# Optimization experiments

Hardware: AMD Instinct MI355X
Metric: run time of the kernel (lower is better)

## Reference

```python
import jax, jax.numpy as jnp
import numpy as np

D_MODEL = 1024
N_HEADS = 16
HEAD_DIM = D_MODEL // N_HEADS
B, S = 4, 2048


def setup_inputs() -> dict:
    key = jax.random.key(0)
    ks = jax.random.split(key, 11)
    scale = 1.0 / np.sqrt(D_MODEL)
    inp = {
        "query": jax.random.normal(ks[0], (B, S, D_MODEL), jnp.float32),
        "key": jax.random.normal(ks[1], (B, S, D_MODEL), jnp.float32),
        "value": jax.random.normal(ks[2], (B, S, D_MODEL), jnp.float32),
        "Wq": jax.random.normal(ks[3], (D_MODEL, D_MODEL), jnp.float32) * scale,
        "bq": jnp.zeros((D_MODEL,), jnp.float32),
        "Wk": jax.random.normal(ks[4], (D_MODEL, D_MODEL), jnp.float32) * scale,
        "bk": jnp.zeros((D_MODEL,), jnp.float32),
        "Wv": jax.random.normal(ks[5], (D_MODEL, D_MODEL), jnp.float32) * scale,
        "bv": jnp.zeros((D_MODEL,), jnp.float32),
        "Wo": jax.random.normal(ks[6], (D_MODEL, D_MODEL), jnp.float32) * scale,
        "bo": jnp.zeros((D_MODEL,), jnp.float32),
    }
    return inp


def _split_heads(x):
    b, s, _ = x.shape
    return x.reshape(b, s, N_HEADS, HEAD_DIM).transpose(0, 2, 1, 3)  # b h s d


def reference(query, key, value, Wq, bq, Wk, bk, Wv, bv, Wo, bo):
    Q = _split_heads(query @ Wq.T + bq)
    K = _split_heads(key @ Wk.T + bk)
    V = _split_heads(value @ Wv.T + bv)
    scale = 1.0 / jnp.sqrt(jnp.float32(HEAD_DIM))
    energy = jnp.einsum("bhqd,bhkd->bhqk", Q, K) * scale  # full N x N scores
    attn = jax.nn.softmax(energy, axis=-1)
    x = jnp.einsum("bhqk,bhkd->bhqd", attn, V)
    x = x.transpose(0, 2, 1, 3).reshape(query.shape[0], -1, D_MODEL)
    return x @ Wo.T + bo
```

## Files before the change

### kernel.cpp

```cpp
#include <hip/hip_runtime.h>
#include <cstdint>
#include <cstddef>


typedef unsigned short u16;
typedef unsigned u32;
typedef short short8 __attribute__((ext_vector_type(8)));
typedef __bf16 bf16x8 __attribute__((ext_vector_type(8)));
typedef float f32x4 __attribute__((ext_vector_type(4)));
typedef float f32x16 __attribute__((ext_vector_type(16)));
typedef unsigned short u16x4 __attribute__((ext_vector_type(4)));
typedef unsigned u32x2 __attribute__((ext_vector_type(2)));
typedef unsigned u32x4 __attribute__((ext_vector_type(4)));
typedef int iv2 __attribute__((ext_vector_type(2)));

__device__ __forceinline__ u16 f2bf(float f) {
  unsigned u = __builtin_bit_cast(unsigned, f);
  u += 0x7fffu + ((u >> 16) & 1u);
  return (u16)(u >> 16);
}
__device__ __forceinline__ bf16x8 bc8(short8 v) { return __builtin_bit_cast(bf16x8, v); }
__device__ __forceinline__ u32 pk_bf16(float a, float b) {
  u32 r;
  asm("v_cvt_pk_bf16_f32 %0, %1, %2" : "=v"(r) : "v"(a), "v"(b));
  return r;
}
__device__ __forceinline__ void gload16(const u16* g, u16* l) {
  __builtin_amdgcn_global_load_lds((const __attribute__((address_space(1))) void*)g,
                                   (__attribute__((address_space(3))) void*)l, 16, 0, 0);
}

__global__ __launch_bounds__(256) void cvt_all(const float* __restrict__ q,
                                               const float* __restrict__ k,
                                               const float* __restrict__ v,
                                               const float* __restrict__ wq,
                                               const float* __restrict__ wk,
                                               const float* __restrict__ wv,
                                               const float* __restrict__ wo,
                                               u16* __restrict__ xq, u16* __restrict__ xk,
                                               u16* __restrict__ xv, u16* __restrict__ wqb,
                                               u16* __restrict__ wkb, u16* __restrict__ wvb,
                                               u16* __restrict__ wob) {
  const size_t i4 = (size_t)blockIdx.x * 256 + threadIdx.x;
  const size_t A4 = 1ull << 21, W4 = 1ull << 18;
  const float* s;
  u16* d;
  size_t off;
  if (i4 < 3 * A4) {
    const int r = (int)(i4 >> 21);
    off = i4 & (A4 - 1);
    s = r == 0 ? q : (r == 1 ? k : v);
    d = r == 0 ? xq : (r == 1 ? xk : xv);
  } else {
    const size_t t = i4 - 3 * A4;
    const int r = (int)(t >> 18);
    off = t & (W4 - 1);
    s = r == 0 ? wq : (r == 1 ? wk : (r == 2 ? wv : wo));
    d = r == 0 ? wqb : (r == 1 ? wkb : (r == 2 ? wvb : wob));
  }
  const f32x4 a = ((const f32x4*)s)[off];
  u32x2 o = {pk_bf16(a[0], a[1]), pk_bf16(a[2], a[3])};
  ((u32x2*)d)[off] = o;
}

__device__ __forceinline__ bf16x8 ldf(const u16* buf, int row, int g) {
  return bc8(*(const short8*)(buf + row * 32 + g * 8));
}

__device__ __forceinline__ void gemm_core(u16* lds, const u16* __restrict__ A,
                                          const u16* __restrict__ Bw,
                                          const float* __restrict__ bias,
                                          void* __restrict__ C, int mode, float oscale) {
  const int t = threadIdx.x;
  const int w = t >> 6, l = t & 63, g = l >> 4, m = l & 15;
  const int wr = w >> 1, wc = w & 1;
  const int m0 = blockIdx.x * 128, n0 = blockIdx.y * 256;
  const u16* gA = A + (size_t)m0 * 1024;
  const u16* gB = Bw + (size_t)n0 * 1024;

  f32x4 acc[4][8];
  const f32x4 z = {0.f, 0.f, 0.f, 0.f};
#pragma unroll
  for (int i = 0; i < 4; ++i)
#pragma unroll
    for (int j = 0; j < 8; ++j) acc[i][j] = z;

#pragma unroll
  for (int tt = 0; tt < 2; ++tt) {
    u16* sA = lds + tt * 12288;
    u16* sB = sA + 4096;
    const int ko = tt * 32;
#pragma unroll
    for (int r = 0; r < 2; ++r) {
      const int c = r * 256 + t;
      gload16(gA + (size_t)(c >> 2) * 1024 + (c & 3) * 8 + ko, sA + c * 8);
    }
#pragma unroll
    for (int r = 0; r < 4; ++r) {
      const int c = r * 256 + t;
      gload16(gB + (size_t)(c >> 2) * 1024 + (c & 3) * 8 + ko, sB + c * 8);
    }
  }
  asm volatile("s_waitcnt vmcnt(6)" ::: "memory");
  __builtin_amdgcn_s_barrier();

  bf16x8 af[4], bfr[8];
  int cb = 0;
  for (int tt = 0; tt < 32; ++tt) {
    u16* bA = lds + cb * 12288;
    u16* bB = bA + 4096;
    const int sbi = (cb == 0) ? 2 : cb - 1;
    u16* sA = lds + sbi * 12288;
    u16* sB = sA + 4096;
    const int ko = (tt + 2) * 32;
    const bool st = tt < 30;

    af[0] = ldf(bA, wr * 64 + m, g);
    af[1] = ldf(bA, wr * 64 + 16 + m, g);
#pragma unroll
    for (int j = 0; j < 4; ++j) bfr[j] = ldf(bB, wc * 128 + j * 16 + m, g);
    if (st) {
#pragma unroll
      for (int r = 0; r < 2; ++r) {
        const int c = r * 256 + t;
        gload16(gA + (size_t)(c >> 2) * 1024 + (c & 3) * 8 + ko, sA + c * 8);
      }
    }
    __builtin_amdgcn_s_barrier();
    __builtin_amdgcn_s_setprio(1);
#pragma unroll
    for (int i = 0; i < 2; ++i)
#pragma unroll
      for (int j = 0; j < 4; ++j)
        acc[i][j] = __builtin_amdgcn_mfma_f32_16x16x32_bf16(af[i], bfr[j], acc[i][j], 0, 0, 0);
    __builtin_amdgcn_s_setprio(0);
    __builtin_amdgcn_s_barrier();

#pragma unroll
    for (int j = 4; j < 8; ++j) bfr[j] = ldf(bB, wc * 128 + j * 16 + m, g);
    if (st) {
#pragma unroll
      for (int r = 0; r < 2; ++r) {
        const int c = r * 256 + t;
        gload16(gB + (size_t)(c >> 2) * 1024 + (c & 3) * 8 + ko, sB + c * 8);
      }
    }
    __builtin_amdgcn_s_barrier();
    __builtin_amdgcn_s_setprio(1);
#pragma unroll
    for (int i = 0; i < 2; ++i)
#pragma unroll
      for (int j = 4; j < 8; ++j)
        acc[i][j] = __builtin_amdgcn_mfma_f32_16x16x32_bf16(af[i], bfr[j], acc[i][j], 0, 0, 0);
    __builtin_amdgcn_s_setprio(0);
    __builtin_amdgcn_s_barrier();

    af[2] = ldf(bA, wr * 64 + 32 + m, g);
    af[3] = ldf(bA, wr * 64 + 48 + m, g);
    if (st) {
#pragma unroll
      for (int r = 2; r < 4; ++r) {
        const int c = r * 256 + t;
        gload16(gB + (size_t)(c >> 2) * 1024 + (c & 3) * 8 + ko, sB + c * 8);
      }
    }
    __builtin_amdgcn_s_barrier();
    __builtin_amdgcn_s_setprio(1);
#pragma unroll
    for (int i = 2; i < 4; ++i)
#pragma unroll
      for (int j = 0; j < 4; ++j)
        acc[i][j] = __builtin_amdgcn_mfma_f32_16x16x32_bf16(af[i], bfr[j], acc[i][j], 0, 0, 0);
    __builtin_amdgcn_s_setprio(0);
    __builtin_amdgcn_s_barrier();

    __builtin_amdgcn_s_setprio(1);
#pragma unroll
    for (int i = 2; i < 4; ++i)
#pragma unroll
      for (int j = 4; j < 8; ++j)
        acc[i][j] = __builtin_amdgcn_mfma_f32_16x16x32_bf16(af[i], bfr[j], acc[i][j], 0, 0, 0);
    __builtin_amdgcn_s_setprio(0);
    if (tt < 30)
      asm volatile("s_waitcnt vmcnt(6)" ::: "memory");
    else
      asm volatile("s_waitcnt vmcnt(0)" ::: "memory");
    __builtin_amdgcn_s_barrier();
    cb = (cb == 2) ? 0 : cb + 1;
  }

  float bv[8];
#pragma unroll
  for (int j = 0; j < 8; ++j) bv[j] = bias[n0 + wc * 128 + j * 16 + m];

  if (mode == 2) {
#pragma unroll
    for (int i = 0; i < 4; ++i)
#pragma unroll
      for (int j = 0; j < 8; ++j) {
        const int row0 = m0 + wr * 64 + i * 16 + g * 4;
        const int col = n0 + wc * 128 + j * 16 + m;
        u16x4 o;
#pragma unroll
        for (int r = 0; r < 4; ++r) o[r] = f2bf((acc[i][j][r] + bv[j]) * oscale);
        *(u16x4*)((u16*)C + ((size_t)(row0 >> 11) * 1024 + col) * 2048 + (row0 & 2047)) = o;
      }
  } else {
#pragma unroll
    for (int i = 0; i < 4; ++i) {
#pragma unroll
      for (int r = 0; r < 4; ++r) {
        const int row = m0 + wr * 64 + i * 16 + g * 4 + r;
#pragma unroll
        for (int j = 0; j < 8; ++j) {
          const int col = n0 + wc * 128 + j * 16 + m;
          const float v = (acc[i][j][r] + bv[j]) * oscale;
          if (mode == 0)
            ((float*)C)[(size_t)row * 1024 + col] = v;
          else
            ((u16*)C)[(size_t)row * 1024 + col] = f2bf(v);
        }
      }
    }
  }
}

__global__ __launch_bounds__(256, 2) void qkv_gemm(const u16* __restrict__ xq,
                                                   const u16* __restrict__ xk,
                                                   const u16* __restrict__ xv,
                                                   const u16* __restrict__ wqb,
                                                   const u16* __restrict__ wkb,
                                                   const u16* __restrict__ wvb,
                                                   const float* __restrict__ bq,
                                                   const float* __restrict__ bk,
                                                   const float* __restrict__ bv,
                                                   u16* __restrict__ Qp, u16* __restrict__ Kp,
                                                   u16* __restrict__ Vt, float SC) {
  __shared__ alignas(16) u16 lds[36864];
  const int z = blockIdx.z;
  const u16* A = z == 0 ? xq : (z == 1 ? xk : xv);
  const u16* W = z == 0 ? wqb : (z == 1 ? wkb : wvb);
  const float* bi = z == 0 ? bq : (z == 1 ? bk : bv);
  void* C = z == 0 ? (void*)Qp : (z == 1 ? (void*)Kp : (void*)Vt);
  gemm_core(lds, A, W, bi, C, z == 2 ? 2 : 1, z == 0 ? SC : 1.f);
}

__global__ __launch_bounds__(256, 2) void o_gemm(const u16* __restrict__ Xa,
                                                 const u16* __restrict__ wob,
                                                 const float* __restrict__ bo,
                                                 float* __restrict__ out) {
  __shared__ alignas(16) u16 lds[36864];
  gemm_core(lds, Xa, wob, bo, out, 0, 1.f);
}

__global__ __launch_bounds__(512, 4) void attn_fwd(const u16* __restrict__ Q,
                                                   const u16* __restrict__ Kp,
                                                   const u16* __restrict__ Vt,
                                                   u16* __restrict__ Xa) {
  __shared__ alignas(16) u16 kl[2][64][72];
  __shared__ alignas(16) u16 vl[2][64][72];
  const int tid = threadIdx.x;
  const int l = tid & 63, w = tid >> 6;
  const int q32 = l & 31, hi = l >> 5;
  const int lin = blockIdx.x + 8 * blockIdx.y;
  const int xp = lin >> 6, yp = lin & 63;
  const int b = yp >> 4, h = yp & 15;
  const int q0 = xp * 256 + w * 32;

  bf16x8 qf[4];
  const size_t qrow = (size_t)b * 2048 + q0 + q32;
#pragma unroll
  for (int ds = 0; ds < 4; ++ds)
    qf[ds] = bc8(*(const short8*)(Q + qrow * 1024 + h * 64 + ds * 16 + hi * 8));

  f32x16 of[2] = {{}, {}};
  float l0 = 0.f, l1 = 0.f, l2 = 0.f, l3 = 0.f;

  const int sr = tid >> 3;
  const int sc8 = (tid & 7) * 8;
  const u16* Kb = Kp + (size_t)b * 2048 * 1024 + h * 64;
  const u16* Vb = Vt + (size_t)yp * 64 * 2048;

  short8 rk = *(const short8*)(Kb + (size_t)sr * 1024 + sc8);
  short8 rv = *(const short8*)(Vb + (size_t)sr * 2048 + sc8);
  *(short8*)(&kl[0][sr][sc8]) = rk;
  *(short8*)(&vl[0][sr][sc8]) = rv;
  rk = *(const short8*)(Kb + (size_t)(64 + sr) * 1024 + sc8);
  rv = *(const short8*)(Vb + (size_t)sr * 2048 + 64 + sc8);
  __syncthreads();

  for (int kt = 0; kt < 32; ++kt) {
    const int cur = kt & 1;

    f32x16 st2[2];
    __builtin_amdgcn_s_setprio(1);
#pragma unroll
    for (int kt2 = 0; kt2 < 2; ++kt2) {
      f32x16 st = {};
#pragma unroll
      for (int ds = 0; ds < 4; ++ds) {
        const bf16x8 kf = bc8(*(const short8*)(&kl[cur][kt2 * 32 + q32][ds * 16 + hi * 8]));
        st = __builtin_amdgcn_mfma_f32_32x32x16_bf16(kf, qf[ds], st, 0, 0, 0);
      }
      st2[kt2] = st;
    }
    __builtin_amdgcn_s_setprio(0);

    if (kt + 1 < 32) {
      *(short8*)(&kl[cur ^ 1][sr][sc8]) = rk;
      *(short8*)(&vl[cur ^ 1][sr][sc8]) = rv;
    }
    if (kt + 2 < 32) {
      rk = *(const short8*)(Kb + (size_t)((kt + 2) * 64 + sr) * 1024 + sc8);
      rv = *(const short8*)(Vb + (size_t)sr * 2048 + (kt + 2) * 64 + sc8);
    }

#pragma unroll
    for (int kt2 = 0; kt2 < 2; ++kt2) {
      float p[16];
#pragma unroll
      for (int r = 0; r < 16; ++r) p[r] = __builtin_amdgcn_exp2f(st2[kt2][r]);
      l0 += (p[0] + p[1]) + (p[2] + p[3]);
      l1 += (p[4] + p[5]) + (p[6] + p[7]);
      l2 += (p[8] + p[9]) + (p[10] + p[11]);
      l3 += (p[12] + p[13]) + (p[14] + p[15]);
#pragma unroll
      for (int s = 0; s < 2; ++s) {
        int X0 = (int)pk_bf16(p[8 * s + 0], p[8 * s + 1]);
        int X1 = (int)pk_bf16(p[8 * s + 2], p[8 * s + 3]);
        int Y0 = (int)pk_bf16(p[8 * s + 4], p[8 * s + 5]);
        int Y1 = (int)pk_bf16(p[8 * s + 6], p[8 * s + 7]);
        iv2 r0 = __builtin_amdgcn_permlane32_swap(X0, Y0, false, false);
        iv2 r1 = __builtin_amdgcn_permlane32_swap(X1, Y1, false, false);
        u32x4 bw = {(u32)r0[0], (u32)r1[0], (u32)r0[1], (u32)r1[1]};
        const bf16x8 pb = __builtin_bit_cast(bf16x8, bw);
        const int ks = kt2 * 2 + s;
        __builtin_amdgcn_s_setprio(1);
#pragma unroll
        for (int dt = 0; dt < 2; ++dt) {
          const bf16x8 vf = bc8(*(const short8*)(&vl[cur][dt * 32 + q32][ks * 16 + hi * 8]));
          of[dt] = __builtin_amdgcn_mfma_f32_32x32x16_bf16(vf, pb, of[dt], 0, 0, 0);
        }
        __builtin_amdgcn_s_setprio(0);
      }
    }
    __syncthreads();
  }

  float lo = (l0 + l1) + (l2 + l3);
  lo += __shfl_xor(lo, 32, 64);
  const float inv = 1.0f / lo;

#pragma unroll
  for (int dt = 0; dt < 2; ++dt)
#pragma unroll
    for (int rg = 0; rg < 4; ++rg) {
      u32x2 o2;
      o2[0] = pk_bf16(of[dt][4 * rg + 0] * inv, of[dt][4 * rg + 1] * inv);
      o2[1] = pk_bf16(of[dt][4 * rg + 2] * inv, of[dt][4 * rg + 3] * inv);
      *(u32x2*)(Xa + qrow * 1024 + h * 64 + dt * 32 + rg * 8 + hi * 4) = o2;
    }
}

extern "C" void kernel_launch(void* const* d_in, const int* in_sizes, int n_in,
                              void* d_out, int out_size, void* d_ws, size_t ws_size,
                              hipStream_t stream) {
  const float* q  = (const float*)d_in[0];
  const float* k  = (const float*)d_in[1];
  const float* v  = (const float*)d_in[2];
  const float* Wq = (const float*)d_in[3];
  const float* bq = (const float*)d_in[4];
  const float* Wk = (const float*)d_in[5];
  const float* bk = (const float*)d_in[6];
  const float* Wv = (const float*)d_in[7];
  const float* bv = (const float*)d_in[8];
  const float* Wo = (const float*)d_in[9];
  const float* bo = (const float*)d_in[10];

  char* ws = (char*)d_ws;
  const size_t MB = 1024ull * 1024ull;
  u16* wqb = (u16*)(ws + 0 * MB);
  u16* wkb = (u16*)(ws + 2 * MB);
  u16* wvb = (u16*)(ws + 4 * MB);
  u16* wob = (u16*)(ws + 6 * MB);
  u16* xq  = (u16*)(ws + 8 * MB);
  u16* xk  = (u16*)(ws + 24 * MB);
  u16* xv  = (u16*)(ws + 40 * MB);
  u16* Qp  = (u16*)(ws + 56 * MB);
  u16* Kp  = (u16*)(ws + 72 * MB);
  u16* Vt  = (u16*)(ws + 88 * MB);
  u16* Xa  = xq;

  cvt_all<<<28672, 256, 0, stream>>>(q, k, v, Wq, Wk, Wv, Wo,
                                     xq, xk, xv, wqb, wkb, wvb, wob);

  const float SC = 0.125f * 1.44269504f;
  qkv_gemm<<<dim3(64, 4, 3), 256, 0, stream>>>(xq, xk, xv, wqb, wkb, wvb,
                                               bq, bk, bv, Qp, Kp, Vt, SC);

  attn_fwd<<<dim3(8, 64), 512, 0, stream>>>(Qp, Kp, Vt, Xa);

  o_gemm<<<dim3(64, 4), 256, 0, stream>>>(Xa, wob, bo, (float*)d_out);
}
```

Baseline: 193.2 us.

## Fuse fp32-to-bf16 activation conversion into QKV GEMM and shrink attention blocks

The QKV GEMM now reads the fp32 activations directly and converts them to bf16 in registers before writing them to LDS. This removes the separate activation conversion pass and its 48MB of bf16 intermediate traffic, leaving only a small weight-conversion kernel. The attention kernel moves from 512-thread blocks to 256-thread blocks with twice as many blocks, each thread loading two K/V rows. The fused path replaces async global-to-LDS loads with register loads plus explicit LDS stores, which may add latency to the GEMM pipeline.

```diff
diff --git a/kernel.cpp b/kernel.cpp
--- a/kernel.cpp
+++ b/kernel.cpp
@@ -30,34 +30,18 @@
                                    (__attribute__((address_space(3))) void*)l, 16, 0, 0);
 }
 
-__global__ __launch_bounds__(256) void cvt_all(const float* __restrict__ q,
-                                               const float* __restrict__ k,
-                                               const float* __restrict__ v,
-                                               const float* __restrict__ wq,
-                                               const float* __restrict__ wk,
-                                               const float* __restrict__ wv,
-                                               const float* __restrict__ wo,
-                                               u16* __restrict__ xq, u16* __restrict__ xk,
-                                               u16* __restrict__ xv, u16* __restrict__ wqb,
-                                               u16* __restrict__ wkb, u16* __restrict__ wvb,
-                                               u16* __restrict__ wob) {
+__global__ __launch_bounds__(256) void cvt_w(const float* __restrict__ wq,
+                                             const float* __restrict__ wk,
+                                             const float* __restrict__ wv,
+                                             const float* __restrict__ wo,
+                                             u16* __restrict__ wqb, u16* __restrict__ wkb,
+                                             u16* __restrict__ wvb, u16* __restrict__ wob) {
   const size_t i4 = (size_t)blockIdx.x * 256 + threadIdx.x;
-  const size_t A4 = 1ull << 21, W4 = 1ull << 18;
-  const float* s;
-  u16* d;
-  size_t off;
-  if (i4 < 3 * A4) {
-    const int r = (int)(i4 >> 21);
-    off = i4 & (A4 - 1);
-    s = r == 0 ? q : (r == 1 ? k : v);
-    d = r == 0 ? xq : (r == 1 ? xk : xv);
-  } else {
-    const size_t t = i4 - 3 * A4;
-    const int r = (int)(t >> 18);
-    off = t & (W4 - 1);
-    s = r == 0 ? wq : (r == 1 ? wk : (r == 2 ? wv : wo));
-    d = r == 0 ? wqb : (r == 1 ? wkb : (r == 2 ? wvb : wob));
-  }
+  const size_t W4 = 1ull << 18;
+  const int r = (int)(i4 >> 18);
+  const size_t off = i4 & (W4 - 1);
+  const float* s = r == 0 ? wq : (r == 1 ? wk : (r == 2 ? wv : wo));
+  u16* d = r == 0 ? wqb : (r == 1 ? wkb : (r == 2 ? wvb : wob));
   const f32x4 a = ((const f32x4*)s)[off];
   u32x2 o = {pk_bf16(a[0], a[1]), pk_bf16(a[2], a[3])};
   ((u32x2*)d)[off] = o;
@@ -67,7 +51,8 @@
   return bc8(*(const short8*)(buf + row * 32 + g * 8));
 }
 
-__device__ __forceinline__ void gemm_core(u16* lds, const u16* __restrict__ A,
+template <int AF32>
+__device__ __forceinline__ void gemm_core(u16* lds, const void* __restrict__ Araw,
                                           const u16* __restrict__ Bw,
                                           const float* __restrict__ bias,
                                           void* __restrict__ C, int mode, float oscale) {
@@ -75,8 +60,10 @@
   const int w = t >> 6, l = t & 63, g = l >> 4, m = l & 15;
   const int wr = w >> 1, wc = w & 1;
   const int m0 = blockIdx.x * 128, n0 = blockIdx.y * 256;
-  const u16* gA = A + (size_t)m0 * 1024;
   const u16* gB = Bw + (size_t)n0 * 1024;
+  const u16* gA16 = (const u16*)Araw + (size_t)m0 * 1024;
+  const float* gAf = (const float*)Araw + (size_t)(m0 + (t >> 1)) * 1024 + (t & 1) * 16;
+  const int awoff = (t >> 1) * 32 + (t & 1) * 16;
 
   f32x4 acc[4][8];
   const f32x4 z = {0.f, 0.f, 0.f, 0.f};
@@ -85,23 +72,54 @@
 #pragma unroll
     for (int j = 0; j < 8; ++j) acc[i][j] = z;
 
-#pragma unroll
-  for (int tt = 0; tt < 2; ++tt) {
-    u16* sA = lds + tt * 12288;
-    u16* sB = sA + 4096;
-    const int ko = tt * 32;
-#pragma unroll
-    for (int r = 0; r < 2; ++r) {
-      const int c = r * 256 + t;
-      gload16(gA + (size_t)(c >> 2) * 1024 + (c & 3) * 8 + ko, sA + c * 8);
-    }
-#pragma unroll
-    for (int r = 0; r < 4; ++r) {
-      const int c = r * 256 + t;
-      gload16(gB + (size_t)(c >> 2) * 1024 + (c & 3) * 8 + ko, sB + c * 8);
-    }
-  }
-  asm volatile("s_waitcnt vmcnt(6)" ::: "memory");
+  if constexpr (AF32) {
+    f32x4 a0[4], a1[4];
+#pragma unroll
+    for (int i = 0; i < 4; ++i) a0[i] = *(const f32x4*)(gAf + i * 4);
+#pragma unroll
+    for (int i = 0; i < 4; ++i) a1[i] = *(const f32x4*)(gAf + 32 + i * 4);
+#pragma unroll
+    for (int tt = 0; tt < 2; ++tt) {
+      u16* sB = lds + tt * 12288 + 4096;
+      const int ko = tt * 32;
+#pragma unroll
+      for (int r = 0; r < 4; ++r) {
+        const int c = r * 256 + t;
+        gload16(gB + (size_t)(c >> 2) * 1024 + (c & 3) * 8 + ko, sB + c * 8);
+      }
+    }
+    u32x4 w0 = {pk_bf16(a0[0][0], a0[0][1]), pk_bf16(a0[0][2], a0[0][3]),
+                pk_bf16(a0[1][0], a0[1][1]), pk_bf16(a0[1][2], a0[1][3])};
+    u32x4 w1 = {pk_bf16(a0[2][0], a0[2][1]), pk_bf16(a0[2][2], a0[2][3]),
+                pk_bf16(a0[3][0], a0[3][1]), pk_bf16(a0[3][2], a0[3][3])};
+    *(u32x4*)(lds + awoff) = w0;
+    *(u32x4*)(lds + awoff + 8) = w1;
+    u32x4 w2 = {pk_bf16(a1[0][0], a1[0][1]), pk_bf16(a1[0][2], a1[0][3]),
+                pk_bf16(a1[1][0], a1[1][1]), pk_bf16(a1[1][2], a1[1][3])};
+    u32x4 w3 = {pk_bf16(a1[2][0], a1[2][1]), pk_bf16(a1[2][2], a1[2][3]),
+                pk_bf16(a1[3][0], a1[3][1]), pk_bf16(a1[3][2], a1[3][3])};
+    *(u32x4*)(lds + 12288 + awoff) = w2;
+    *(u32x4*)(lds + 12288 + awoff + 8) = w3;
+    asm volatile("s_waitcnt vmcnt(4) lgkmcnt(0)" ::: "memory");
+  } else {
+#pragma unroll
+    for (int tt = 0; tt < 2; ++tt) {
+      u16* sA = lds + tt * 12288;
+      u16* sB = sA + 4096;
+      const int ko = tt * 32;
+#pragma unroll
+      for (int r = 0; r < 2; ++r) {
+        const int c = r * 256 + t;
+        gload16(gA16 + (size_t)(c >> 2) * 1024 + (c & 3) * 8 + ko, sA + c * 8);
+      }
+#pragma unroll
+      for (int r = 0; r < 4; ++r) {
+        const int c = r * 256 + t;
+        gload16(gB + (size_t)(c >> 2) * 1024 + (c & 3) * 8 + ko, sB + c * 8);
+      }
+    }
+    asm volatile("s_waitcnt vmcnt(6)" ::: "memory");
+  }
   __builtin_amdgcn_s_barrier();
 
   bf16x8 af[4], bfr[8];
@@ -119,11 +137,17 @@
     af[1] = ldf(bA, wr * 64 + 16 + m, g);
 #pragma unroll
     for (int j = 0; j < 4; ++j) bfr[j] = ldf(bB, wc * 128 + j * 16 + m, g);
+    f32x4 av[4];
     if (st) {
-#pragma unroll
-      for (int r = 0; r < 2; ++r) {
-        const int c = r * 256 + t;
-        gload16(gA + (size_t)(c >> 2) * 1024 + (c & 3) * 8 + ko, sA + c * 8);
+      if constexpr (AF32) {
+#pragma unroll
+        for (int i = 0; i < 4; ++i) av[i] = *(const f32x4*)(gAf + ko + i * 4);
+      } else {
+#pragma unroll
+        for (int r = 0; r < 2; ++r) {
+          const int c = r * 256 + t;
+          gload16(gA16 + (size_t)(c >> 2) * 1024 + (c & 3) * 8 + ko, sA + c * 8);
+        }
       }
     }
     __builtin_amdgcn_s_barrier();
@@ -181,10 +205,25 @@
       for (int j = 4; j < 8; ++j)
         acc[i][j] = __builtin_amdgcn_mfma_f32_16x16x32_bf16(af[i], bfr[j], acc[i][j], 0, 0, 0);
     __builtin_amdgcn_s_setprio(0);
-    if (tt < 30)
-      asm volatile("s_waitcnt vmcnt(6)" ::: "memory");
-    else
-      asm volatile("s_waitcnt vmcnt(0)" ::: "memory");
+    if constexpr (AF32) {
+      if (st) {
+        asm volatile("s_waitcnt vmcnt(4)" ::: "memory");
+        u32x4 w0 = {pk_bf16(av[0][0], av[0][1]), pk_bf16(av[0][2], av[0][3]),
+                    pk_bf16(av[1][0], av[1][1]), pk_bf16(av[1][2], av[1][3])};
+        u32x4 w1 = {pk_bf16(av[2][0], av[2][1]), pk_bf16(av[2][2], av[2][3]),
+                    pk_bf16(av[3][0], av[3][1]), pk_bf16(av[3][2], av[3][3])};
+        *(u32x4*)(sA + awoff) = w0;
+        *(u32x4*)(sA + awoff + 8) = w1;
+        asm volatile("s_waitcnt lgkmcnt(0)" ::: "memory");
+      } else {
+        asm volatile("s_waitcnt vmcnt(0)" ::: "memory");
+      }
+    } else {
+      if (st)
+        asm volatile("s_waitcnt vmcnt(6)" ::: "memory");
+      else
+        asm volatile("s_waitcnt vmcnt(0)" ::: "memory");
+    }
     __builtin_amdgcn_s_barrier();
     cb = (cb == 2) ? 0 : cb + 1;
   }
@@ -225,9 +264,9 @@
   }
 }
 
-__global__ __launch_bounds__(256, 2) void qkv_gemm(const u16* __restrict__ xq,
-                                                   const u16* __restrict__ xk,
-                                                   const u16* __restrict__ xv,
+__global__ __launch_bounds__(256, 2) void qkv_gemm(const float* __restrict__ q,
+                                                   const float* __restrict__ k,
+                                                   const float* __restrict__ v,
                                                    const u16* __restrict__ wqb,
                                                    const u16* __restrict__ wkb,
                                                    const u16* __restrict__ wvb,
@@ -238,11 +277,11 @@
                                                    u16* __restrict__ Vt, float SC) {
   __shared__ alignas(16) u16 lds[36864];
   const int z = blockIdx.z;
-  const u16* A = z == 0 ? xq : (z == 1 ? xk : xv);
+  const float* A = z == 0 ? q : (z == 1 ? k : v);
   const u16* W = z == 0 ? wqb : (z == 1 ? wkb : wvb);
   const float* bi = z == 0 ? bq : (z == 1 ? bk : bv);
   void* C = z == 0 ? (void*)Qp : (z == 1 ? (void*)Kp : (void*)Vt);
-  gemm_core(lds, A, W, bi, C, z == 2 ? 2 : 1, z == 0 ? SC : 1.f);
+  gemm_core<1>(lds, A, W, bi, C, z == 2 ? 2 : 1, z == 0 ? SC : 1.f);
 }
 
 __global__ __launch_bounds__(256, 2) void o_gemm(const u16* __restrict__ Xa,
@@ -250,10 +289,10 @@
                                                  const float* __restrict__ bo,
                                                  float* __restrict__ out) {
   __shared__ alignas(16) u16 lds[36864];
-  gemm_core(lds, Xa, wob, bo, out, 0, 1.f);
-}
-
-__global__ __launch_bounds__(512, 4) void attn_fwd(const u16* __restrict__ Q,
+  gemm_core<0>(lds, Xa, wob, bo, out, 0, 1.f);
+}
+
+__global__ __launch_bounds__(256, 4) void attn_fwd(const u16* __restrict__ Q,
                                                    const u16* __restrict__ Kp,
                                                    const u16* __restrict__ Vt,
                                                    u16* __restrict__ Xa) {
@@ -262,10 +301,10 @@
   const int tid = threadIdx.x;
   const int l = tid & 63, w = tid >> 6;
   const int q32 = l & 31, hi = l >> 5;
-  const int lin = blockIdx.x + 8 * blockIdx.y;
+  const int lin = blockIdx.x + 16 * blockIdx.y;
   const int xp = lin >> 6, yp = lin & 63;
   const int b = yp >> 4, h = yp & 15;
-  const int q0 = xp * 256 + w * 32;
+  const int q0 = xp * 128 + w * 32;
 
   bf16x8 qf[4];
   const size_t qrow = (size_t)b * 2048 + q0 + q32;
@@ -281,13 +320,22 @@
   const u16* Kb = Kp + (size_t)b * 2048 * 1024 + h * 64;
   const u16* Vb = Vt + (size_t)yp * 64 * 2048;
 
-  short8 rk = *(const short8*)(Kb + (size_t)sr * 1024 + sc8);
-  short8 rv = *(const short8*)(Vb + (size_t)sr * 2048 + sc8);
-  *(short8*)(&kl[0][sr][sc8]) = rk;
-  *(short8*)(&vl[0][sr][sc8]) = rv;
-  rk = *(const short8*)(Kb + (size_t)(64 + sr) * 1024 + sc8);
-  rv = *(const short8*)(Vb + (size_t)sr * 2048 + 64 + sc8);
-  __syncthreads();
+  short8 rk[2], rv[2];
+#pragma unroll
+  for (int it = 0; it < 2; ++it) {
+    const int r = sr + it * 32;
+    rk[it] = *(const short8*)(Kb + (size_t)r * 1024 + sc8);
+    rv[it] = *(const short8*)(Vb + (size_t)r * 2048 + sc8);
+    *(short8*)(&kl[0][r][sc8]) = rk[it];
+    *(short8*)(&vl[0][r][sc8]) = rv[it];
+  }
+#pragma unroll
+  for (int it = 0; it < 2; ++it) {
+    const int r = sr + it * 32;
+    rk[it] = *(const short8*)(Kb + (size_t)(64 + r) * 1024 + sc8);
+    rv[it] = *(const short8*)(Vb + (size_t)r * 2048 + 64 + sc8);
+  }
+  asm volatile("s_waitcnt lgkmcnt(0)\n\ts_barrier" ::: "memory");
 
   for (int kt = 0; kt < 32; ++kt) {
     const int cur = kt & 1;
@@ -307,12 +355,20 @@
     __builtin_amdgcn_s_setprio(0);
 
     if (kt + 1 < 32) {
-      *(short8*)(&kl[cur ^ 1][sr][sc8]) = rk;
-      *(short8*)(&vl[cur ^ 1][sr][sc8]) = rv;
+#pragma unroll
+      for (int it = 0; it < 2; ++it) {
+        const int r = sr + it * 32;
+        *(short8*)(&kl[cur ^ 1][r][sc8]) = rk[it];
+        *(short8*)(&vl[cur ^ 1][r][sc8]) = rv[it];
+      }
     }
     if (kt + 2 < 32) {
-      rk = *(const short8*)(Kb + (size_t)((kt + 2) * 64 + sr) * 1024 + sc8);
-      rv = *(const short8*)(Vb + (size_t)sr * 2048 + (kt + 2) * 64 + sc8);
+#pragma unroll
+      for (int it = 0; it < 2; ++it) {
+        const int r = sr + it * 32;
+        rk[it] = *(const short8*)(Kb + (size_t)((kt + 2) * 64 + r) * 1024 + sc8);
+        rv[it] = *(const short8*)(Vb + (size_t)r * 2048 + (kt + 2) * 64 + sc8);
+      }
     }
 
 #pragma unroll
@@ -344,7 +400,7 @@
         __builtin_amdgcn_s_setprio(0);
       }
     }
-    __syncthreads();
+    asm volatile("s_waitcnt lgkmcnt(0)\n\ts_barrier" ::: "memory");
   }
 
   float lo = (l0 + l1) + (l2 + l3);
@@ -383,22 +439,18 @@
   u16* wkb = (u16*)(ws + 2 * MB);
   u16* wvb = (u16*)(ws + 4 * MB);
   u16* wob = (u16*)(ws + 6 * MB);
-  u16* xq  = (u16*)(ws + 8 * MB);
-  u16* xk  = (u16*)(ws + 24 * MB);
-  u16* xv  = (u16*)(ws + 40 * MB);
-  u16* Qp  = (u16*)(ws + 56 * MB);
-  u16* Kp  = (u16*)(ws + 72 * MB);
-  u16* Vt  = (u16*)(ws + 88 * MB);
-  u16* Xa  = xq;
-
-  cvt_all<<<28672, 256, 0, stream>>>(q, k, v, Wq, Wk, Wv, Wo,
-                                     xq, xk, xv, wqb, wkb, wvb, wob);
+  u16* Xa  = (u16*)(ws + 8 * MB);
+  u16* Qp  = (u16*)(ws + 24 * MB);
+  u16* Kp  = (u16*)(ws + 40 * MB);
+  u16* Vt  = (u16*)(ws + 56 * MB);
+
+  cvt_w<<<4096, 256, 0, stream>>>(Wq, Wk, Wv, Wo, wqb, wkb, wvb, wob);
 
   const float SC = 0.125f * 1.44269504f;
-  qkv_gemm<<<dim3(64, 4, 3), 256, 0, stream>>>(xq, xk, xv, wqb, wkb, wvb,
+  qkv_gemm<<<dim3(64, 4, 3), 256, 0, stream>>>(q, k, v, wqb, wkb, wvb,
                                                bq, bk, bv, Qp, Kp, Vt, SC);
 
-  attn_fwd<<<dim3(8, 64), 512, 0, stream>>>(Qp, Kp, Vt, Xa);
+  attn_fwd<<<dim3(16, 64), 256, 0, stream>>>(Qp, Kp, Vt, Xa);
 
   o_gemm<<<dim3(64, 4), 256, 0, stream>>>(Xa, wob, bo, (float*)d_out);
 }
```

Result: slower. 198.4 us (+2.7%).

## Halve attention block size to 4 waves and double grid size

Applied to the files above, without the earlier changes.

The attention kernel now uses 256-thread blocks that each cover 128 queries instead of 512 threads covering 256, and the grid doubles to 1024 blocks. Each thread loads two K/V rows per tile to keep the shared-memory staging intact. The __syncthreads calls become a raw lgkmcnt wait plus s_barrier, so the barrier no longer waits on outstanding global loads (vmcnt). This targets finer scheduling and lighter barriers, at the cost of loading each K/V tile from global memory twice as often in total.

```diff
diff --git a/kernel.cpp b/kernel.cpp
--- a/kernel.cpp
+++ b/kernel.cpp
@@ -253,7 +253,7 @@
   gemm_core(lds, Xa, wob, bo, out, 0, 1.f);
 }
 
-__global__ __launch_bounds__(512, 4) void attn_fwd(const u16* __restrict__ Q,
+__global__ __launch_bounds__(256, 4) void attn_fwd(const u16* __restrict__ Q,
                                                    const u16* __restrict__ Kp,
                                                    const u16* __restrict__ Vt,
                                                    u16* __restrict__ Xa) {
@@ -262,10 +262,10 @@
   const int tid = threadIdx.x;
   const int l = tid & 63, w = tid >> 6;
   const int q32 = l & 31, hi = l >> 5;
-  const int lin = blockIdx.x + 8 * blockIdx.y;
+  const int lin = blockIdx.x + 16 * blockIdx.y;
   const int xp = lin >> 6, yp = lin & 63;
   const int b = yp >> 4, h = yp & 15;
-  const int q0 = xp * 256 + w * 32;
+  const int q0 = xp * 128 + w * 32;
 
   bf16x8 qf[4];
   const size_t qrow = (size_t)b * 2048 + q0 + q32;
@@ -281,13 +281,22 @@
   const u16* Kb = Kp + (size_t)b * 2048 * 1024 + h * 64;
   const u16* Vb = Vt + (size_t)yp * 64 * 2048;
 
-  short8 rk = *(const short8*)(Kb + (size_t)sr * 1024 + sc8);
-  short8 rv = *(const short8*)(Vb + (size_t)sr * 2048 + sc8);
-  *(short8*)(&kl[0][sr][sc8]) = rk;
-  *(short8*)(&vl[0][sr][sc8]) = rv;
-  rk = *(const short8*)(Kb + (size_t)(64 + sr) * 1024 + sc8);
-  rv = *(const short8*)(Vb + (size_t)sr * 2048 + 64 + sc8);
-  __syncthreads();
+  short8 rk[2], rv[2];
+#pragma unroll
+  for (int it = 0; it < 2; ++it) {
+    const int r = sr + it * 32;
+    rk[it] = *(const short8*)(Kb + (size_t)r * 1024 + sc8);
+    rv[it] = *(const short8*)(Vb + (size_t)r * 2048 + sc8);
+    *(short8*)(&kl[0][r][sc8]) = rk[it];
+    *(short8*)(&vl[0][r][sc8]) = rv[it];
+  }
+#pragma unroll
+  for (int it = 0; it < 2; ++it) {
+    const int r = sr + it * 32;
+    rk[it] = *(const short8*)(Kb + (size_t)(64 + r) * 1024 + sc8);
+    rv[it] = *(const short8*)(Vb + (size_t)r * 2048 + 64 + sc8);
+  }
+  asm volatile("s_waitcnt lgkmcnt(0)\n\ts_barrier" ::: "memory");
 
   for (int kt = 0; kt < 32; ++kt) {
     const int cur = kt & 1;
@@ -307,12 +316,20 @@
     __builtin_amdgcn_s_setprio(0);
 
     if (kt + 1 < 32) {
-      *(short8*)(&kl[cur ^ 1][sr][sc8]) = rk;
-      *(short8*)(&vl[cur ^ 1][sr][sc8]) = rv;
+#pragma unroll
+      for (int it = 0; it < 2; ++it) {
+        const int r = sr + it * 32;
+        *(short8*)(&kl[cur ^ 1][r][sc8]) = rk[it];
+        *(short8*)(&vl[cur ^ 1][r][sc8]) = rv[it];
+      }
     }
     if (kt + 2 < 32) {
-      rk = *(const short8*)(Kb + (size_t)((kt + 2) * 64 + sr) * 1024 + sc8);
-      rv = *(const short8*)(Vb + (size_t)sr * 2048 + (kt + 2) * 64 + sc8);
+#pragma unroll
+      for (int it = 0; it < 2; ++it) {
+        const int r = sr + it * 32;
+        rk[it] = *(const short8*)(Kb + (size_t)((kt + 2) * 64 + r) * 1024 + sc8);
+        rv[it] = *(const short8*)(Vb + (size_t)r * 2048 + (kt + 2) * 64 + sc8);
+      }
     }
 
 #pragma unroll
@@ -344,7 +361,7 @@
         __builtin_amdgcn_s_setprio(0);
       }
     }
-    __syncthreads();
+    asm volatile("s_waitcnt lgkmcnt(0)\n\ts_barrier" ::: "memory");
   }
 
   float lo = (l0 + l1) + (l2 + l3);
@@ -398,7 +415,7 @@
   qkv_gemm<<<dim3(64, 4, 3), 256, 0, stream>>>(xq, xk, xv, wqb, wkb, wvb,
                                                bq, bk, bv, Qp, Kp, Vt, SC);
 
-  attn_fwd<<<dim3(8, 64), 512, 0, stream>>>(Qp, Kp, Vt, Xa);
+  attn_fwd<<<dim3(16, 64), 256, 0, stream>>>(Qp, Kp, Vt, Xa);
 
   o_gemm<<<dim3(64, 4), 256, 0, stream>>>(Xa, wob, bo, (float*)d_out);
 }
```

Result: slower. 200.9 us (+4.0%).
